# Optimization experiments

Hardware: AMD Instinct MI355X
Metric: run time of the kernel (lower is better)

## Reference

```python
import jax, jax.numpy as jnp
import numpy as np

# config matching init_kwargs: stox_params=[4,2,1,1,64,2], in=64, out=128, k=3, pad=1
A_BITS = 4          # a_slices = a_bits / a_bits_per_stream = 4
W_SLICES = 2        # w_bits / w_bits_per_slice = 2
NUM_CHUNKS = 9      # ceil(64*9/64)
SUB = 64            # crossbar chunk width
ITERS = 2           # stochastic iterations
EPS = 1e-5          # BatchNorm1d eps


def ste(y, x):
    # straight-through estimator: forward y, backward identity of x
    return x + jax.lax.stop_gradient(y - x)


def unfold3x3(x):
    # torch F.unfold(x, 3, dilation=1, padding=1, stride=1): [B,C,H,W] -> [B, C*9, H*W]
    B, C, H, W = x.shape
    xp = jnp.pad(x, ((0, 0), (0, 0), (1, 1), (1, 1)))
    cols = [xp[:, :, i:i + H, j:j + W] for i in range(3) for j in range(3)]
    return jnp.stack(cols, axis=2).reshape(B, C * 9, H * W)  # (c, kh, kw) ordering


def setup_inputs() -> dict:
    key = jax.random.key(0)
    k1, k2 = jax.random.split(key)
    inputs = jax.random.normal(k1, (8, 64, 32, 32), jnp.float32)
    fan_in = 64 * 9  # kaiming_normal_ fan_in
    weight = jax.random.normal(k2, (128 * W_SLICES, 64, 3, 3), jnp.float32) * np.float32(np.sqrt(2.0 / fan_in))
    bn_gamma = jnp.ones((128 * W_SLICES,), jnp.float32)
    bn_beta = jnp.zeros((128 * W_SLICES,), jnp.float32)
    return {"inputs": inputs, "weight": weight, "bn_gamma": bn_gamma, "bn_beta": bn_beta}


def reference(inputs, weight, bn_gamma, bn_beta):
    O = weight.shape[0]  # out_channels * W_SLICES = 256
    # --- per-output-row weight standardization + 1-bit STE quantization (WeightQuantize) ---
    wf = weight.reshape(O, -1)                       # [O, Cin*9]
    bw = wf - wf.mean(-1, keepdims=True)
    bw = bw / bw.std(-1, ddof=1, keepdims=True)      # torch std is unbiased
    qw = ste(jnp.sign(bw), bw)                       # [O, Cin*9]
    # --- unfold + multi-bit input stream (create_input_stream): bit-planes stacked on batch dim ---
    a = unfold3x3(inputs)                            # [B, Cin*9, L]
    Bsz, C9, L = a.shape
    x = jnp.clip(a, 0.0, 1.0)
    q = jnp.round(x * (2 ** A_BITS - 1))
    bits = jnp.stack([jnp.floor(q / (2 ** i)) % 2 for i in range(A_BITS)], 0)  # [A,B,C9,L]
    qa = bits.reshape(A_BITS * Bsz, C9, L)
    # --- chunked crossbar linear + BatchNorm1d(train) + MTJ sign, summed over chunks/iterations ---
    out = jnp.zeros((A_BITS * Bsz, O, L), a.dtype)
    for c in range(NUM_CHUNKS):
        wk = qa[:, c * SUB:(c + 1) * SUB, :]         # [B', SUB, L]
        ww = qw[:, c * SUB:(c + 1) * SUB]            # [O, SUB]
        for _ in range(ITERS):
            lin = jnp.einsum('bcl,oc->bol', wk, ww)  # [B', O, L]
            mu = lin.mean((0, 2), keepdims=True)
            var = lin.var((0, 2), keepdims=True)     # biased, as torch BN training
            bn = bn_gamma[None, :, None] * (lin - mu) / jnp.sqrt(var + EPS) + bn_beta[None, :, None]
            out = out + ste(jnp.sign(bn), bn)        # MTJ stochastic comparator -> sign w/ STE
    # --- bit-weighted reconstructions ---
    wvec = (2.0 ** jnp.arange(W_SLICES, dtype=a.dtype)) / (2 ** W_SLICES - 1)
    out = jnp.einsum('s,bsol->bol', wvec, out.reshape(A_BITS * Bsz, W_SLICES, O // W_SLICES, L))
    avec = (2.0 ** jnp.arange(A_BITS, dtype=a.dtype)) / (2 ** A_BITS - 1)
    out = jnp.einsum('a,abol->bol', avec, out.reshape(A_BITS, Bsz, O // W_SLICES, L))
    # --- F.fold with (1,1) kernel == reshape to square spatial map ---
    P = int(np.sqrt(L))
    return out.reshape(Bsz, O // W_SLICES, P, P)
```

## Files before the change

### kernel.cpp

```cpp
#include <hip/hip_runtime.h>
#include <cstdint>
#include <cstddef>

static const size_t OFF_ACT  = 0;
static const size_t OFF_W    = OFF_ACT + 2359296;
static const size_t OFF_T    = OFF_W   + 18432;
static const size_t OFF_NS1  = OFF_T   + 18432;
static const size_t OFF_MUG  = OFF_NS1 + 9216;
static const size_t OFF_FLAG = OFF_MUG + 18432;
static const size_t OFF_WB   = OFF_FLAG + 1024;
static const size_t OFF_CQ   = OFF_WB + 147456;
static const size_t OFF_FF   = OFF_CQ + 9216;

typedef int v4i __attribute__((ext_vector_type(4)));

__device__ __forceinline__ int isgn(int e) {
  int t = e < -1 ? -1 : e;
  return t > 1 ? 1 : t;
}

__global__ __launch_bounds__(256) void k_prep(const float* __restrict__ x,
                                              const float* __restrict__ w,
                                              const float* __restrict__ gamma,
                                              const float* __restrict__ beta,
                                              int* __restrict__ T,
                                              uint64_t* __restrict__ act,
                                              uint64_t* __restrict__ wbits,
                                              int* __restrict__ flag,
                                              signed char* __restrict__ wbyte,
                                              int* __restrict__ flagF) {
  int bid = blockIdx.x;
  int tid = threadIdx.x;
  if (bid < 512) {
    int base = bid << 10;
    int vals[9];
#pragma unroll
    for (int k = 0; k < 9; ++k) vals[k] = 0;
#pragma unroll
    for (int i = 0; i < 4; ++i) {
      int px = tid + i * 256;
      int h = px >> 5, ww = px & 31;
      float v = x[base + px];
      v = fminf(fmaxf(v, 0.f), 1.f);
      int q = (int)rintf(v * 15.f);
      int pc = __popc((unsigned)q);
      vals[0] += pc;
      if (h == 0) vals[1] += pc;
      if (h == 31) vals[2] += pc;
      if (ww == 0) vals[3] += pc;
      if (ww == 31) vals[4] += pc;
      if (h == 0 && ww == 0) vals[5] += pc;
      if (h == 0 && ww == 31) vals[6] += pc;
      if (h == 31 && ww == 0) vals[7] += pc;
      if (h == 31 && ww == 31) vals[8] += pc;
    }
#pragma unroll
    for (int k = 0; k < 9; ++k)
      for (int off = 32; off; off >>= 1) vals[k] += __shfl_down(vals[k], off, 64);
    __shared__ int red[4][9];
    int wid = tid >> 6, lane = tid & 63;
    if (lane == 0)
#pragma unroll
      for (int k = 0; k < 9; ++k) red[wid][k] = vals[k];
    __syncthreads();
    if (tid < 9) T[bid * 9 + tid] = red[0][tid] + red[1][tid] + red[2][tid] + red[3][tid];
  } else if (bid < 1664) {
    int blk = bid - 512;
    int bc = blk >> 4;
    int c = bc % 9, b = bc / 9;
    int l0 = (blk & 15) << 6;
    int h0 = l0 >> 5;
    int chLo = (c * 64) / 9;
    __shared__ unsigned char qlds[8][4][34];
    for (int e = tid; e < 1024; e += 256) {
      int ci = e >> 7, rem = e & 127, ri = rem >> 5, wi = rem & 31;
      int hh = h0 - 1 + ri;
      int qv = 0;
      if ((unsigned)hh < 32u) {
        float v = x[((b * 64 + chLo + ci) << 10) + (hh << 5) + wi];
        v = fminf(fmaxf(v, 0.f), 1.f);
        qv = (int)rintf(v * 15.f);
      }
      qlds[ci][ri][wi + 1] = (unsigned char)qv;
      if (wi == 0) qlds[ci][ri][0] = 0;
      if (wi == 31) qlds[ci][ri][33] = 0;
    }
    __syncthreads();

    int half = tid & 3;
    int dl = tid >> 2;
    int l = l0 + dl;
    int h = l >> 5, w0 = l & 31;
    int hr = h - h0;
    int i9 = c * 64 + half * 16;
    int ch = i9 / 9;
    int k = i9 - ch * 9;
    int ki = k / 3, kj = k - ki * 3;
    int cch = ch - chLo;
    unsigned m0 = 0, m1 = 0, m2 = 0, m3 = 0;
#pragma unroll
    for (int jj = 0; jj < 16; ++jj) {
      int q = qlds[cch][hr + ki][w0 + kj];
      m0 |= (unsigned)(q & 1) << jj;
      m1 |= (unsigned)((q >> 1) & 1) << jj;
      m2 |= (unsigned)((q >> 2) & 1) << jj;
      m3 |= (unsigned)((q >> 3) & 1) << jj;
      if (++kj == 3) { kj = 0; if (++ki == 3) { ki = 0; ++cch; } }
    }
    size_t stride = 8 * 9 * 1024;
    size_t off = ((size_t)b * 9 + c) * 1024 + l;
    unsigned short* a16 = (unsigned short*)act;
    a16[(0 * stride + off) * 4 + half] = (unsigned short)m0;
    a16[(1 * stride + off) * 4 + half] = (unsigned short)m1;
    a16[(2 * stride + off) * 4 + half] = (unsigned short)m2;
    a16[(3 * stride + off) * 4 + half] = (unsigned short)m3;
  } else {
    int lane = tid & 63;
    int wid = tid >> 6;
    int o = (bid - 1664) * 4 + wid;
    const float* row = w + (size_t)o * 576;
    double s = 0.0;
#pragma unroll
    for (int i = 0; i < 9; ++i) s += (double)row[lane + i * 64];
    for (int off = 32; off; off >>= 1) s += __shfl_down(s, off, 64);
    s = __shfl(s, 0, 64);
    float mean = (float)(s / 576.0);
#pragma unroll
    for (int c = 0; c < 9; ++c) {
      float v = row[c * 64 + lane];
      int pos = (v - mean) > 0.f;
      unsigned long long m = __ballot(pos);
      if (lane == 0) wbits[o * 9 + c] = (uint64_t)m;
      wbyte[(c * 256 + o) * 64 + lane] = pos ? (signed char)1 : (signed char)-1;
    }
    if (lane == 0) {
      int f = (beta[o] == 0.f && gamma[o] > 0.f) ? 1 : 0;
      flag[o] = f;
      flagF[o] = f;
    }
  }
}

__global__ __launch_bounds__(256) void k_s1(const int* __restrict__ T,
                                            const uint64_t* __restrict__ wbits,
                                            const int* __restrict__ flag,
                                            const float* __restrict__ gamma,
                                            const uint64_t* __restrict__ act,
                                            int* __restrict__ negS1,
                                            int* __restrict__ cq,
                                            int* __restrict__ flagF,
                                            float2* __restrict__ MUG) {
  __shared__ int Tsh[576];
  __shared__ int Ush[9 * 65];
  int tid = threadIdx.x;
  for (int i = tid; i < 576; i += 256) {
    int acc = 0;
#pragma unroll
    for (int b = 0; b < 8; ++b) acc += T[b * 576 + i];
    Tsh[i] = acc;
  }
  __syncthreads();
  for (int i = tid; i < 576; i += 256) {
    int ch = i / 9;
    int k = i - ch * 9;
    int ki = k / 3, kj = k - ki * 3;
    const int* t = &Tsh[ch * 9];
    int u = t[0];
    if (ki == 0) u -= t[2]; else if (ki == 2) u -= t[1];
    if (kj == 0) u -= t[4]; else if (kj == 2) u -= t[3];
    if (ki == 0 && kj == 0) u += t[8];
    if (ki == 0 && kj == 2) u += t[7];
    if (ki == 2 && kj == 0) u += t[6];
    if (ki == 2 && kj == 2) u += t[5];
    Ush[(i >> 6) * 65 + (i & 63)] = u;
  }
  __syncthreads();
  int pair = blockIdx.x * 256 + tid;
  int o = pair / 9, c = pair - o * 9;
  uint64_t wv = wbits[pair];
  int tot = 0, pos = 0;
#pragma unroll 8
  for (int j = 0; j < 64; ++j) {
    int cnt = Ush[c * 65 + j];
    tot += cnt;
    if ((wv >> j) & 1) pos += cnt;
  }
  int s1 = 2 * pos - tot;
  negS1[c * 256 + o] = -s1;
  cq[c * 256 + o] = -(s1 >> 15);
  if ((s1 & 32767) == 0) atomicAnd(&flagF[o], 0);
  if (!flag[o]) {
    int s2 = 0;
    for (int i = 0; i < 32768; ++i) {
      uint64_t av = act[((size_t)(i >> 10) * 9 + c) * 1024 + (i & 1023)];
      int lin = 2 * __popcll(av & wv) - __popcll(av);
      s2 += lin * lin;
    }
    float mu = (float)s1 * (1.f / 32768.f);
    float ex2 = (float)s2 * (1.f / 32768.f);
    float var = ex2 - mu * mu;
    if (var < 0.f) var = 0.f;
    MUG[pair] = make_float2(mu, gamma[o] / sqrtf(var + 1e-5f));
  }
}

__global__ __launch_bounds__(512, 4) void k_out(const uint64_t* __restrict__ act,
                                                const signed char* __restrict__ wbyte,
                                                const int* __restrict__ negS1g,
                                                const int* __restrict__ cqg,
                                                const float2* __restrict__ MUG,
                                                const int* __restrict__ flag,
                                                const int* __restrict__ flagF,
                                                const float* __restrict__ beta,
                                                float* __restrict__ out) {
  __shared__ __align__(16) int cqsh[2304];
  __shared__ unsigned int part[4][16][65];
  int tid = threadIdx.x;
  int lt = blockIdx.x;
  int b = blockIdx.y;
  for (int i = tid; i < 2304; i += 512) cqsh[i] = cqg[i];
  __syncthreads();

  int lane = tid & 63;
  int w8 = __builtin_amdgcn_readfirstlane(tid >> 6);
  int w = w8 & 3;
  int hi = w8 >> 2;
  int row = lane & 15;
  int g = lane >> 4;
  int sh16 = (g & 1) * 16;
  int aBase = 2 * hi;

  int o0 = w * 32 + (lane & 31);
  int fb = flagF[o0] & flagF[o0 + 128];
  bool fastAll = (bool)__all(fb != 0);

  const v4i zacc = {0, 0, 0, 0};
  int l = lt * 16 + row;
  const char* actbyte = (const char*)act + ((size_t)b * 9 * 1024 + l) * 8 + (g >> 1) * 4;

  unsigned pt[16];

  if (fastAll) {
    int P[4][4];
#pragma unroll
    for (int q = 0; q < 4; ++q)
#pragma unroll
      for (int r = 0; r < 4; ++r) P[q][r] = 0;

    for (int c = 0; c < 9; ++c) {
      v4i Af[4], Cin[4];
#pragma unroll
      for (int q = 0; q < 4; ++q) {
        int ot = 2 * w + (q & 1) + (q >> 1) * 8;
        Af[q] = *(const v4i*)(wbyte + ((size_t)(c * 256 + ot * 16 + row) * 64 + g * 16));
        Cin[q] = *(const v4i*)&cqsh[c * 256 + ot * 16 + g * 4];
      }
      unsigned dwv[2];
#pragma unroll
      for (int ai = 0; ai < 2; ++ai)
        dwv[ai] = *(const unsigned*)(actbyte +
                                     (size_t)(aBase + ai) * 589824 +
                                     (size_t)c * 8192);

      int pc[4][4];
#pragma unroll
      for (int q = 0; q < 4; ++q)
#pragma unroll
        for (int r = 0; r < 4; ++r) pc[q][r] = 0;

#pragma unroll
      for (int ai2 = 0; ai2 < 2; ++ai2) {
        int ai = 1 - ai2;
        unsigned bits = (dwv[ai] >> sh16) & 0xFFFFu;
        v4i Bf;
#pragma unroll
        for (int d = 0; d < 4; ++d)
          Bf[d] = (int)((((bits >> (4 * d)) & 0xFu) * 0x00204081u) & 0x01010101u);
#pragma unroll
        for (int q = 0; q < 4; ++q) {
          v4i acc = __builtin_amdgcn_mfma_i32_16x16x64_i8(Af[q], Bf, Cin[q], 0, 0, 0);
#pragma unroll
          for (int r = 0; r < 4; ++r)
            pc[q][r] += pc[q][r] + (acc[r] > 0 ? 1 : 0);
        }
      }
#pragma unroll
      for (int q = 0; q < 4; ++q)
#pragma unroll
        for (int r = 0; r < 4; ++r) P[q][r] += pc[q][r];
    }
#pragma unroll
    for (int q = 0; q < 4; ++q)
#pragma unroll
      for (int r = 0; r < 4; ++r) pt[q * 4 + r] = (unsigned)P[q][r];
  } else {
    int M2[2][4] = {{0, 0, 0, 0}, {0, 0, 0, 0}};
    float F2[2][4] = {{0.f, 0.f, 0.f, 0.f}, {0.f, 0.f, 0.f, 0.f}};
    int flv[4][4];
#pragma unroll
    for (int q = 0; q < 4; ++q) {
      int ot = 2 * w + (q & 1) + (q >> 1) * 8;
#pragma unroll
      for (int r = 0; r < 4; ++r) flv[q][r] = flag[ot * 16 + g * 4 + r];
    }
    for (int c = 0; c < 9; ++c) {
      v4i Af[4];
      int nS[4][4];
#pragma unroll
      for (int q = 0; q < 4; ++q) {
        int ot = 2 * w + (q & 1) + (q >> 1) * 8;
        Af[q] = *(const v4i*)(wbyte + ((size_t)(c * 256 + ot * 16 + row) * 64 + g * 16));
#pragma unroll
        for (int r = 0; r < 4; ++r) nS[q][r] = negS1g[c * 256 + ot * 16 + g * 4 + r];
      }
      unsigned dwv[2];
#pragma unroll
      for (int ai = 0; ai < 2; ++ai)
        dwv[ai] = *(const unsigned*)(actbyte +
                                     (size_t)(aBase + ai) * 589824 +
                                     (size_t)c * 8192);
#pragma unroll
      for (int ai = 0; ai < 2; ++ai) {
        unsigned bits = (dwv[ai] >> sh16) & 0xFFFFu;
        v4i Bf;
#pragma unroll
        for (int d = 0; d < 4; ++d)
          Bf[d] = (int)((((bits >> (4 * d)) & 0xFu) * 0x00204081u) & 0x01010101u);
#pragma unroll
        for (int q = 0; q < 4; ++q) {
          v4i acc = __builtin_amdgcn_mfma_i32_16x16x64_i8(Af[q], Bf, zacc, 0, 0, 0);
          int ot = 2 * w + (q & 1) + (q >> 1) * 8;
#pragma unroll
          for (int r = 0; r < 4; ++r) {
            int lin = acc[r];
            if (flv[q][r]) {
              M2[q & 1][r] += isgn((lin << 15) + nS[q][r]) << (ai + (q >> 1));
            } else {
              int o = ot * 16 + g * 4 + r;
              float2 m2 = MUG[o * 9 + c];
              float bn = m2.y * ((float)lin - m2.x) + beta[o];
              float sg = (bn > 0.f) ? 1.f : ((bn < 0.f) ? -1.f : 0.f);
              F2[q & 1][r] += sg * (float)(1 << (ai + (q >> 1)));
            }
          }
        }
      }
    }
#pragma unroll
    for (int q2 = 0; q2 < 2; ++q2)
#pragma unroll
      for (int r = 0; r < 4; ++r) {
        pt[q2 * 4 + r] = (unsigned)M2[q2][r];
        pt[8 + q2 * 4 + r] = __float_as_uint(F2[q2][r]);
      }
  }

  if (hi) {
#pragma unroll
    for (int i = 0; i < 16; ++i) part[w][i][lane] = pt[i];
  }
  __syncthreads();
  if (!hi) {
    if (fastAll) {
      int Pf[4][4];
#pragma unroll
      for (int q = 0; q < 4; ++q)
#pragma unroll
        for (int r = 0; r < 4; ++r)
          Pf[q][r] = (int)pt[q * 4 + r] + 4 * (int)part[w][q * 4 + r][lane];
#pragma unroll
      for (int q2 = 0; q2 < 2; ++q2)
#pragma unroll
        for (int r = 0; r < 4; ++r) {
          int oo = (2 * w + q2) * 16 + g * 4 + r;
          int M = 2 * (Pf[q2][r] + 2 * Pf[q2 + 2][r]) - 405;
          out[((size_t)b * 128 + oo) * 1024 + l] = (float)M * (2.f / 45.f);
        }
    } else {
#pragma unroll
      for (int q2 = 0; q2 < 2; ++q2)
#pragma unroll
        for (int r = 0; r < 4; ++r) {
          int oo = (2 * w + q2) * 16 + g * 4 + r;
          int Mf = (int)pt[q2 * 4 + r] + 4 * (int)part[w][q2 * 4 + r][lane];
          float Ff = __uint_as_float(pt[8 + q2 * 4 + r]) +
                     4.f * __uint_as_float(part[w][8 + q2 * 4 + r][lane]);
          out[((size_t)b * 128 + oo) * 1024 + l] =
              ((float)Mf + Ff) * (2.f / 45.f);
        }
    }
  }
}

extern "C" void kernel_launch(void* const* d_in, const int* in_sizes, int n_in,
                              void* d_out, int out_size, void* d_ws, size_t ws_size,
                              hipStream_t stream) {
  const float* inputs = (const float*)d_in[0];
  const float* weight = (const float*)d_in[1];
  const float* gamma = (const float*)d_in[2];
  const float* beta = (const float*)d_in[3];
  float* out = (float*)d_out;

  char* ws = (char*)d_ws;
  uint64_t* act = (uint64_t*)(ws + OFF_ACT);
  uint64_t* wbits = (uint64_t*)(ws + OFF_W);
  int* T = (int*)(ws + OFF_T);
  int* negS1 = (int*)(ws + OFF_NS1);
  float2* MUG = (float2*)(ws + OFF_MUG);
  int* flag = (int*)(ws + OFF_FLAG);
  signed char* wbyte = (signed char*)(ws + OFF_WB);
  int* cq = (int*)(ws + OFF_CQ);
  int* flagF = (int*)(ws + OFF_FF);

  k_prep<<<1728, 256, 0, stream>>>(inputs, weight, gamma, beta, T, act, wbits, flag, wbyte, flagF);
  k_s1<<<9, 256, 0, stream>>>(T, wbits, flag, gamma, act, negS1, cq, flagF, MUG);
  k_out<<<dim3(64, 8), 512, 0, stream>>>(act, wbyte, negS1, cq, MUG, flag, flagF, beta, out);
}
```

Before: 88.11 us.

## Fuse per-channel statistics kernel into output kernel via redundant per-block compute

Removes the separate k_s1 launch and has every k_out block recompute the per-(channel,chunk) sums, flags and BN parameters into shared memory. This saves a kernel launch and the global round trip for negS1/cq/flagF/MUG. In exchange, each of 512 blocks redundantly does the 2304-pair reduction, and the slow-path variance loop over 32768 elements would run in every block. Shared memory usage also grows by about 30KB per block, which may cut occupancy.

```diff
diff --git a/kernel.cpp b/kernel.cpp
--- a/kernel.cpp
+++ b/kernel.cpp
@@ -5,12 +5,8 @@
 static const size_t OFF_ACT  = 0;
 static const size_t OFF_W    = OFF_ACT + 2359296;
 static const size_t OFF_T    = OFF_W   + 18432;
-static const size_t OFF_NS1  = OFF_T   + 18432;
-static const size_t OFF_MUG  = OFF_NS1 + 9216;
-static const size_t OFF_FLAG = OFF_MUG + 18432;
+static const size_t OFF_FLAG = OFF_T   + 18432;
 static const size_t OFF_WB   = OFF_FLAG + 1024;
-static const size_t OFF_CQ   = OFF_WB + 147456;
-static const size_t OFF_FF   = OFF_CQ + 9216;
 
 typedef int v4i __attribute__((ext_vector_type(4)));
 
@@ -27,8 +23,7 @@
                                               uint64_t* __restrict__ act,
                                               uint64_t* __restrict__ wbits,
                                               int* __restrict__ flag,
-                                              signed char* __restrict__ wbyte,
-                                              int* __restrict__ flagF) {
+                                              signed char* __restrict__ wbyte) {
   int bid = blockIdx.x;
   int tid = threadIdx.x;
   if (bid < 512) {
@@ -133,34 +128,38 @@
       if (lane == 0) wbits[o * 9 + c] = (uint64_t)m;
       wbyte[(c * 256 + o) * 64 + lane] = pos ? (signed char)1 : (signed char)-1;
     }
-    if (lane == 0) {
-      int f = (beta[o] == 0.f && gamma[o] > 0.f) ? 1 : 0;
-      flag[o] = f;
-      flagF[o] = f;
-    }
+    if (lane == 0) flag[o] = (beta[o] == 0.f && gamma[o] > 0.f) ? 1 : 0;
   }
 }
 
-__global__ __launch_bounds__(256) void k_s1(const int* __restrict__ T,
-                                            const uint64_t* __restrict__ wbits,
-                                            const int* __restrict__ flag,
-                                            const float* __restrict__ gamma,
-                                            const uint64_t* __restrict__ act,
-                                            int* __restrict__ negS1,
-                                            int* __restrict__ cq,
-                                            int* __restrict__ flagF,
-                                            float2* __restrict__ MUG) {
+__global__ __launch_bounds__(512, 4) void k_out(const uint64_t* __restrict__ act,
+                                                const uint64_t* __restrict__ wbits,
+                                                const signed char* __restrict__ wbyte,
+                                                const int* __restrict__ T,
+                                                const int* __restrict__ flag,
+                                                const float* __restrict__ gamma,
+                                                const float* __restrict__ beta,
+                                                float* __restrict__ out) {
   __shared__ int Tsh[576];
   __shared__ int Ush[9 * 65];
+  __shared__ __align__(16) int cqsh[2304];
+  __shared__ int nS1sh[2304];
+  __shared__ int flagFsh[256];
+  __shared__ float2 MUGsh[2304];
+  __shared__ unsigned int part[4][16][65];
   int tid = threadIdx.x;
-  for (int i = tid; i < 576; i += 256) {
+  int lt = blockIdx.x;
+  int b = blockIdx.y;
+
+  for (int i = tid; i < 576; i += 512) {
     int acc = 0;
 #pragma unroll
-    for (int b = 0; b < 8; ++b) acc += T[b * 576 + i];
+    for (int bb = 0; bb < 8; ++bb) acc += T[bb * 576 + i];
     Tsh[i] = acc;
   }
+  for (int o = tid; o < 256; o += 512) flagFsh[o] = flag[o];
   __syncthreads();
-  for (int i = tid; i < 576; i += 256) {
+  for (int i = tid; i < 576; i += 512) {
     int ch = i / 9;
     int k = i - ch * 9;
     int ki = k / 3, kj = k - ki * 3;
@@ -175,50 +174,34 @@
     Ush[(i >> 6) * 65 + (i & 63)] = u;
   }
   __syncthreads();
-  int pair = blockIdx.x * 256 + tid;
-  int o = pair / 9, c = pair - o * 9;
-  uint64_t wv = wbits[pair];
-  int tot = 0, pos = 0;
+  for (int pair = tid; pair < 2304; pair += 512) {
+    int o = pair / 9, c = pair - o * 9;
+    uint64_t wv = wbits[pair];
+    int tot = 0, pos = 0;
 #pragma unroll 8
-  for (int j = 0; j < 64; ++j) {
-    int cnt = Ush[c * 65 + j];
-    tot += cnt;
-    if ((wv >> j) & 1) pos += cnt;
-  }
-  int s1 = 2 * pos - tot;
-  negS1[c * 256 + o] = -s1;
-  cq[c * 256 + o] = -(s1 >> 15);
-  if ((s1 & 32767) == 0) atomicAnd(&flagF[o], 0);
-  if (!flag[o]) {
-    int s2 = 0;
-    for (int i = 0; i < 32768; ++i) {
-      uint64_t av = act[((size_t)(i >> 10) * 9 + c) * 1024 + (i & 1023)];
-      int lin = 2 * __popcll(av & wv) - __popcll(av);
-      s2 += lin * lin;
-    }
-    float mu = (float)s1 * (1.f / 32768.f);
-    float ex2 = (float)s2 * (1.f / 32768.f);
-    float var = ex2 - mu * mu;
-    if (var < 0.f) var = 0.f;
-    MUG[pair] = make_float2(mu, gamma[o] / sqrtf(var + 1e-5f));
-  }
-}
-
-__global__ __launch_bounds__(512, 4) void k_out(const uint64_t* __restrict__ act,
-                                                const signed char* __restrict__ wbyte,
-                                                const int* __restrict__ negS1g,
-                                                const int* __restrict__ cqg,
-                                                const float2* __restrict__ MUG,
-                                                const int* __restrict__ flag,
-                                                const int* __restrict__ flagF,
-                                                const float* __restrict__ beta,
-                                                float* __restrict__ out) {
-  __shared__ __align__(16) int cqsh[2304];
-  __shared__ unsigned int part[4][16][65];
-  int tid = threadIdx.x;
-  int lt = blockIdx.x;
-  int b = blockIdx.y;
-  for (int i = tid; i < 2304; i += 512) cqsh[i] = cqg[i];
+    for (int j = 0; j < 64; ++j) {
+      int cnt = Ush[c * 65 + j];
+      tot += cnt;
+      if ((wv >> j) & 1) pos += cnt;
+    }
+    int s1 = 2 * pos - tot;
+    nS1sh[c * 256 + o] = -s1;
+    cqsh[c * 256 + o] = -(s1 >> 15);
+    if ((s1 & 32767) == 0) atomicAnd(&flagFsh[o], 0);
+    if (!flag[o]) {
+      int s2 = 0;
+      for (int i = 0; i < 32768; ++i) {
+        uint64_t av = act[((size_t)(i >> 10) * 9 + c) * 1024 + (i & 1023)];
+        int lin = 2 * __popcll(av & wv) - __popcll(av);
+        s2 += lin * lin;
+      }
+      float mu = (float)s1 * (1.f / 32768.f);
+      float ex2 = (float)s2 * (1.f / 32768.f);
+      float var = ex2 - mu * mu;
+      if (var < 0.f) var = 0.f;
+      MUGsh[pair] = make_float2(mu, gamma[o] / sqrtf(var + 1e-5f));
+    }
+  }
   __syncthreads();
 
   int lane = tid & 63;
@@ -231,7 +214,7 @@
   int aBase = 2 * hi;
 
   int o0 = w * 32 + (lane & 31);
-  int fb = flagF[o0] & flagF[o0 + 128];
+  int fb = flagFsh[o0] & flagFsh[o0 + 128];
   bool fastAll = (bool)__all(fb != 0);
 
   const v4i zacc = {0, 0, 0, 0};
@@ -311,7 +294,7 @@
         int ot = 2 * w + (q & 1) + (q >> 1) * 8;
         Af[q] = *(const v4i*)(wbyte + ((size_t)(c * 256 + ot * 16 + row) * 64 + g * 16));
 #pragma unroll
-        for (int r = 0; r < 4; ++r) nS[q][r] = negS1g[c * 256 + ot * 16 + g * 4 + r];
+        for (int r = 0; r < 4; ++r) nS[q][r] = nS1sh[c * 256 + ot * 16 + g * 4 + r];
       }
       unsigned dwv[2];
 #pragma unroll
@@ -337,7 +320,7 @@
               M2[q & 1][r] += isgn((lin << 15) + nS[q][r]) << (ai + (q >> 1));
             } else {
               int o = ot * 16 + g * 4 + r;
-              float2 m2 = MUG[o * 9 + c];
+              float2 m2 = MUGsh[o * 9 + c];
               float bn = m2.y * ((float)lin - m2.x) + beta[o];
               float sg = (bn > 0.f) ? 1.f : ((bn < 0.f) ? -1.f : 0.f);
               F2[q & 1][r] += sg * (float)(1 << (ai + (q >> 1)));
@@ -405,14 +388,9 @@
   uint64_t* act = (uint64_t*)(ws + OFF_ACT);
   uint64_t* wbits = (uint64_t*)(ws + OFF_W);
   int* T = (int*)(ws + OFF_T);
-  int* negS1 = (int*)(ws + OFF_NS1);
-  float2* MUG = (float2*)(ws + OFF_MUG);
   int* flag = (int*)(ws + OFF_FLAG);
   signed char* wbyte = (signed char*)(ws + OFF_WB);
-  int* cq = (int*)(ws + OFF_CQ);
-  int* flagF = (int*)(ws + OFF_FF);
-
-  k_prep<<<1728, 256, 0, stream>>>(inputs, weight, gamma, beta, T, act, wbits, flag, wbyte, flagF);
-  k_s1<<<9, 256, 0, stream>>>(T, wbits, flag, gamma, act, negS1, cq, flagF, MUG);
-  k_out<<<dim3(64, 8), 512, 0, stream>>>(act, wbyte, negS1, cq, MUG, flag, flagF, beta, out);
+
+  k_prep<<<1728, 256, 0, stream>>>(inputs, weight, gamma, beta, T, act, wbits, flag, wbyte);
+  k_out<<<dim3(64, 8), 512, 0, stream>>>(act, wbits, wbyte, T, flag, gamma, beta, out);
 }
```

Measured after the change: 94.89 us. 7.7% more time.
